# Kernel tuning notes

Measured on AMD Instinct MI355X. Metric: run time of the kernel, lower is better.

Reference implementation:

```python
import jax, jax.numpy as jnp
import numpy as np

B, N, DM, H = 2, 512, 1024, 16  # batch, seq, d_model, n_heads
DEPTHS = [1, 2, 4, 8]
LAM = 0.1  # lambda_distance


def setup_inputs() -> dict:
    key = jax.random.key(0)
    ks = jax.random.split(key, 2 + 5 * len(DEPTHS))
    inp = {
        "x": jax.random.normal(ks[0], (B, N, DM), jnp.float32),
        "depth_logits": jax.random.normal(ks[1], (len(DEPTHS),), jnp.float32),
    }
    j = 2
    for i, D in enumerate(DEPTHS):
        ds = DM // D
        r = max(1, D // 4)
        inp[f"pe{i}"] = jax.random.normal(ks[j], (N, D, ds), jnp.float32) * 0.02; j += 1
        inp[f"wqkv{i}"] = jax.random.normal(ks[j], (D, ds, 3 * ds), jnp.float32) / np.sqrt(ds); j += 1
        inp[f"wo{i}"] = jax.random.normal(ks[j], (DM, DM), jnp.float32) / np.sqrt(DM); j += 1
        inp[f"fu{i}"] = jax.random.normal(ks[j], (D, r), jnp.float32) / np.sqrt(r); j += 1
        inp[f"fv{i}"] = jax.random.normal(ks[j], (r, D), jnp.float32); j += 1
    return inp


def _ring_bias(n, lam, dtype):
    # toroidal (circular) distance bias on the sequence ring, normalized by N/2
    idx = jnp.arange(n)
    diff = jnp.abs(idx[:, None] - idx[None, :])
    ring = jnp.minimum(diff, n - diff).astype(dtype)
    return -lam * ring * (2.0 / n)  # [N, N]


def _toroidal_branch(x, pe, wqkv, wo, fu, fv):
    # x: [B, N, DM]; pe: [N, D, ds]; wqkv: [D, ds, 3ds]; wo: [DM, DM]; fu@fv: [D, D]
    b, n, dm = x.shape
    d_depth, ds, _ = wqkv.shape
    hd = ds // H
    xs = x.reshape(b, n, d_depth, ds) + pe[None]          # [B, N, D, ds]
    qkv = jnp.einsum('bnds,dse->bnde', xs, wqkv)          # per-depth-slice projection
    q, k, v = jnp.split(qkv, 3, axis=-1)
    q = q.reshape(b, n, d_depth, H, hd)
    k = k.reshape(b, n, d_depth, H, hd)
    v = v.reshape(b, n, d_depth, H, hd)
    bias = _ring_bias(n, LAM, x.dtype)
    scores = jnp.einsum('bndhe,bmdhe->bdhnm', q, k) / jnp.sqrt(jnp.asarray(hd, x.dtype))
    attn = jax.nn.softmax(scores + bias, axis=-1)          # [B, D, H, N, N]
    o = jnp.einsum('bdhnm,bmdhe->bndhe', attn, v).reshape(b, n, d_depth, ds)
    mix = fu @ fv                                          # low-rank depth fusion [D, D]
    fused = jnp.einsum('df,bnfs->bnds', mix, o).reshape(b, n, dm)
    return fused @ wo


def _forward(x, depth_logits, pe0, wqkv0, wo0, fu0, fv0, pe1, wqkv1, wo1, fu1, fv1,
             pe2, wqkv2, wo2, fu2, fv2, pe3, wqkv3, wo3, fu3, fv3):
    # inference-mode depth selection: hard one-hot at argmax (all branches still computed)
    w = jax.nn.one_hot(jnp.argmax(depth_logits), depth_logits.shape[0], dtype=x.dtype)
    params = [(pe0, wqkv0, wo0, fu0, fv0), (pe1, wqkv1, wo1, fu1, fv1),
              (pe2, wqkv2, wo2, fu2, fv2), (pe3, wqkv3, wo3, fu3, fv3)]
    out = jnp.zeros_like(x)
    for i, p in enumerate(params):
        out = out + w[i] * _toroidal_branch(x, *p)
    return out


def reference(x, depth_logits, pe0, wqkv0, wo0, fu0, fv0, pe1, wqkv1, wo1, fu1, fv1,
              pe2, wqkv2, wo2, fu2, fv2, pe3, wqkv3, wo3, fu3, fv3):
    return _forward(x, depth_logits, pe0, wqkv0, wo0, fu0, fv0, pe1, wqkv1, wo1, fu1, fv1,
                    pe2, wqkv2, wo2, fu2, fv2, pe3, wqkv3, wo3, fu3, fv3)
```

## Files before the change

### kernel.cpp

```cpp
#include <hip/hip_runtime.h>

#define B_   2
#define N_   512
#define DM_  1024
#define H_   16
#define LAM_ 0.1f

typedef __attribute__((ext_vector_type(8))) short bf16x8;
typedef __attribute__((ext_vector_type(4))) float f32x4;
typedef unsigned short ush;
struct ush4 { ush x, y, z, w; };
struct uint2s { unsigned x, y; };

__device__ inline ush f2bf(float v) {
    union { float f; unsigned u; } c; c.f = v;
    unsigned r = c.u + 0x7FFF + ((c.u >> 16) & 1);
    return (ush)(r >> 16);
}
__device__ inline float bf2f(ush b) {
    union { float f; unsigned u; } c; c.u = ((unsigned)b) << 16; return c.f;
}
__device__ inline f32x4 mfma16(bf16x8 a, bf16x8 b, f32x4 c) {
    return __builtin_amdgcn_mfma_f32_16x16x32_bf16(a, b, c, 0, 0, 0);
}

__global__ void k_select(const float* __restrict__ logits, int* __restrict__ sel) {
    if (threadIdx.x == 0) {
        float best = logits[0]; int bi = 0;
        for (int i = 1; i < 4; ++i) { float v = logits[i]; if (v > best) { best = v; bi = i; } }
        *sel = bi;
    }
}

template<int D>
__device__ void prep_wt_tile(int bT, int tid, const float* __restrict__ w,
                             ush* __restrict__ wh, ush* __restrict__ wl,
                             float (*lds)[65]) {
    constexpr int ds = DM_ / D;
    constexpr int tpr = 3 * ds / 64;
    constexpr int tpc = ds / 64;
    constexpr int tpd = tpr * tpc;
    if (bT >= D * tpd) return;
    const int d = bT / tpd, rem = bT % tpd;
    const int tr = rem / tpr, tc = rem % tpr;
    const float* src = w + (size_t)d * ds * 3 * ds;
    ush* dsth = wh + (size_t)d * 3 * ds * ds;
    ush* dstl = wl + (size_t)d * 3 * ds * ds;
    const int c = tid & 63, r0 = tid >> 6;
    #pragma unroll
    for (int j = 0; j < 16; ++j) {
        const int r = j * 4 + r0;
        lds[r][c] = src[(size_t)(tr * 64 + r) * (3 * ds) + tc * 64 + c];
    }
    __syncthreads();
    #pragma unroll
    for (int j = 0; j < 16; ++j) {
        const int r = j * 4 + r0;
        const float v = lds[c][r];
        const size_t o = (size_t)(tc * 64 + r) * ds + tr * 64 + c;
        const ush h = f2bf(v);
        dsth[o] = h; dstl[o] = f2bf(v - bf2f(h));
    }
}
__global__ __launch_bounds__(256) void k_prep(
        const int* __restrict__ sel, const float* __restrict__ x,
        const float* __restrict__ pe0, const float* __restrict__ pe1,
        const float* __restrict__ pe2, const float* __restrict__ pe3,
        const float* __restrict__ w0, const float* __restrict__ w1,
        const float* __restrict__ w2, const float* __restrict__ w3,
        const float* __restrict__ wo0, const float* __restrict__ wo1,
        const float* __restrict__ wo2, const float* __restrict__ wo3,
        ush* __restrict__ xh, ush* __restrict__ xl,
        ush* __restrict__ wqh, ush* __restrict__ wql,
        ush* __restrict__ woh, ush* __restrict__ wol) {
    __shared__ float lds[64][65];
    const int s = *sel;
    const int bid = blockIdx.x, tid = threadIdx.x;
    if (bid < 1024) {
        const float* pe = (s == 0) ? pe0 : (s == 1) ? pe1 : (s == 2) ? pe2 : pe3;
        const size_t i0 = ((size_t)bid * 256 + tid) * 4;
        const float4 xv = *(const float4*)&x[i0];
        const float4 pv = *(const float4*)&pe[i0 & ((size_t)N_ * DM_ - 1)];
        ush4 h4, l4;
        float v;
        v = xv.x + pv.x; h4.x = f2bf(v); l4.x = f2bf(v - bf2f(h4.x));
        v = xv.y + pv.y; h4.y = f2bf(v); l4.y = f2bf(v - bf2f(h4.y));
        v = xv.z + pv.z; h4.z = f2bf(v); l4.z = f2bf(v - bf2f(h4.z));
        v = xv.w + pv.w; h4.w = f2bf(v); l4.w = f2bf(v - bf2f(h4.w));
        *(ush4*)&xh[i0] = h4;
        *(ush4*)&xl[i0] = l4;
    } else if (bid < 1792) {
        const int bT = bid - 1024;
        switch (s) {
            case 0: prep_wt_tile<1>(bT, tid, w0, wqh, wql, lds); break;
            case 1: prep_wt_tile<2>(bT, tid, w1, wqh, wql, lds); break;
            case 2: prep_wt_tile<4>(bT, tid, w2, wqh, wql, lds); break;
            case 3: prep_wt_tile<8>(bT, tid, w3, wqh, wql, lds); break;
        }
    } else {
        const float* w = (s == 0) ? wo0 : (s == 1) ? wo1 : (s == 2) ? wo2 : wo3;
        const int bT = bid - 1792;
        const int tr = bT >> 4, tc = bT & 15;
        const int c = tid & 63, r0 = tid >> 6;
        #pragma unroll
        for (int j = 0; j < 16; ++j) {
            const int r = j * 4 + r0;
            lds[r][c] = w[(size_t)(tr * 64 + r) * DM_ + tc * 64 + c];
        }
        __syncthreads();
        #pragma unroll
        for (int j = 0; j < 16; ++j) {
            const int r = j * 4 + r0;
            const float v = lds[c][r];
            const size_t o = (size_t)(tc * 64 + r) * DM_ + tr * 64 + c;
            const ush h = f2bf(v);
            woh[o] = h; wol[o] = f2bf(v - bf2f(h));
        }
    }
}

template<int KD>
__device__ void gemm_core(const ush* __restrict__ Ah, const ush* __restrict__ Al, int lda,
                          const ush* __restrict__ Bh, const ush* __restrict__ Bl, int ldb,
                          int row0, int col0, int tid, ush* lds, f32x4 acc[2][2]) {
    ush* lAh = lds; ush* lAl = lds + 2560; ush* lBh = lds + 5120; ush* lBl = lds + 7680;
    const int srow = tid >> 2, scg = tid & 3;
    const int lane = tid & 63, w = tid >> 6;
    const int wm = w >> 1, wn = w & 1;
    const int lr = lane & 15, lb = lane >> 4;

    for (int k0 = 0; k0 < KD; k0 += 32) {
        *(bf16x8*)&lAh[srow * 40 + scg * 8] =
            *(const bf16x8*)&Ah[(size_t)(row0 + srow) * lda + k0 + scg * 8];
        *(bf16x8*)&lAl[srow * 40 + scg * 8] =
            *(const bf16x8*)&Al[(size_t)(row0 + srow) * lda + k0 + scg * 8];
        *(bf16x8*)&lBh[srow * 40 + scg * 8] =
            *(const bf16x8*)&Bh[(size_t)(col0 + srow) * ldb + k0 + scg * 8];
        *(bf16x8*)&lBl[srow * 40 + scg * 8] =
            *(const bf16x8*)&Bl[(size_t)(col0 + srow) * ldb + k0 + scg * 8];
        __syncthreads();
        bf16x8 ah[2], al[2], bh[2], bl[2];
        #pragma unroll
        for (int mg = 0; mg < 2; ++mg) {
            const int r = wm * 32 + mg * 16 + lr;
            ah[mg] = *(const bf16x8*)&lAh[r * 40 + lb * 8];
            al[mg] = *(const bf16x8*)&lAl[r * 40 + lb * 8];
        }
        #pragma unroll
        for (int ng = 0; ng < 2; ++ng) {
            const int r = wn * 32 + ng * 16 + lr;
            bh[ng] = *(const bf16x8*)&lBh[r * 40 + lb * 8];
            bl[ng] = *(const bf16x8*)&lBl[r * 40 + lb * 8];
        }
        #pragma unroll
        for (int mg = 0; mg < 2; ++mg)
            #pragma unroll
            for (int ng = 0; ng < 2; ++ng) {
                acc[mg][ng] = mfma16(ah[mg], bh[ng], acc[mg][ng]);
                acc[mg][ng] = mfma16(al[mg], bh[ng], acc[mg][ng]);
                acc[mg][ng] = mfma16(ah[mg], bl[ng], acc[mg][ng]);
            }
        __syncthreads();
    }
}

template<int D>
__device__ void qkv_body(int bid, int tid,
                         const ush* __restrict__ xh, const ush* __restrict__ xl,
                         const ush* __restrict__ wh, const ush* __restrict__ wl,
                         ush* __restrict__ Qh, ush* __restrict__ Ql,
                         ush* __restrict__ Kh, ush* __restrict__ Kl,
                         ush* __restrict__ Vth, ush* __restrict__ Vtl, ush* lds) {
    constexpr int ds = DM_ / D;
    constexpr int hd = ds / H_;
    constexpr int nx = 3 * ds / 64;
    const int bx = bid % nx, by = (bid / nx) & 7, bz = bid / (nx * 8);
    const int b = bz / D, d = bz % D;
    const int row0 = by * 64, col0 = bx * 64;

    f32x4 acc[2][2] = {};
    gemm_core<ds>(xh + (size_t)b * N_ * DM_ + d * ds, xl + (size_t)b * N_ * DM_ + d * ds, DM_,
                  wh + (size_t)d * 3 * ds * ds, wl + (size_t)d * 3 * ds * ds, ds,
                  row0, col0, tid, lds, acc);

    const int lane = tid & 63, w = tid >> 6;
    const int wm = w >> 1, wn = w & 1;
    const int lr = lane & 15, lb = lane >> 4;
    #pragma unroll
    for (int mg = 0; mg < 2; ++mg)
        #pragma unroll
        for (int ng = 0; ng < 2; ++ng) {
            const int n0 = row0 + wm * 32 + mg * 16 + lb * 4;
            const int e  = col0 + wn * 32 + ng * 16 + lr;
            const int part = e / ds, ep = e % ds;
            const int h = ep / hd, t = ep % hd;
            const size_t head = ((size_t)b * D + d) * H_ + h;
            if (part == 2) {
                ush4 h4, l4;
                const float v0 = acc[mg][ng][0], v1 = acc[mg][ng][1];
                const float v2 = acc[mg][ng][2], v3 = acc[mg][ng][3];
                h4.x = f2bf(v0); l4.x = f2bf(v0 - bf2f(h4.x));
                h4.y = f2bf(v1); l4.y = f2bf(v1 - bf2f(h4.y));
                h4.z = f2bf(v2); l4.z = f2bf(v2 - bf2f(h4.z));
                h4.w = f2bf(v3); l4.w = f2bf(v3 - bf2f(h4.w));
                const size_t o = (head * hd + t) * N_ + n0;
                *(ush4*)&Vth[o] = h4;
                *(ush4*)&Vtl[o] = l4;
            } else {
                #pragma unroll
                for (int i = 0; i < 4; ++i) {
                    const size_t o = (head * N_ + n0 + i) * hd + t;
                    const float v = acc[mg][ng][i];
                    const ush hh = f2bf(v), ll = f2bf(v - bf2f(hh));
                    if (part == 0) { Qh[o] = hh; Ql[o] = ll; }
                    else           { Kh[o] = hh; Kl[o] = ll; }
                }
            }
        }
}
__global__ __launch_bounds__(256) void k_qkv(
        const int* __restrict__ sel,
        const ush* __restrict__ xh, const ush* __restrict__ xl,
        const ush* __restrict__ wh, const ush* __restrict__ wl,
        ush* __restrict__ Qh, ush* __restrict__ Ql,
        ush* __restrict__ Kh, ush* __restrict__ Kl,
        ush* __restrict__ Vth, ush* __restrict__ Vtl) {
    __shared__ ush lds[4 * 2560];
    const int bid = blockIdx.x, tid = threadIdx.x;
    switch (*sel) {
        case 0: qkv_body<1>(bid, tid, xh, xl, wh, wl, Qh, Ql, Kh, Kl, Vth, Vtl, lds); break;
        case 1: qkv_body<2>(bid, tid, xh, xl, wh, wl, Qh, Ql, Kh, Kl, Vth, Vtl, lds); break;
        case 2: qkv_body<4>(bid, tid, xh, xl, wh, wl, Qh, Ql, Kh, Kl, Vth, Vtl, lds); break;
        case 3: qkv_body<8>(bid, tid, xh, xl, wh, wl, Qh, Ql, Kh, Kl, Vth, Vtl, lds); break;
    }
}

template<int D>
__device__ void attn_body(int bid, int tid,
        const ush* __restrict__ Qh, const ush* __restrict__ Ql,
        const ush* __restrict__ Kh, const ush* __restrict__ Kl,
        const ush* __restrict__ Vth, const ush* __restrict__ Vtl,
        float* __restrict__ O, ush* Pbase) {
    constexpr int ds = DM_ / D, hd = ds / H_;
    constexpr int CH = (hd >= 64) ? 2 : 1;
    constexpr int NT = (hd >= 16) ? hd / 16 : 1;
    constexpr int NBLK = B_ * D * H_ * 8;
    if (bid >= NBLK) return;
    const int bidr = (bid & 7) * (NBLK / 8) + (bid >> 3);
    const int w = tid >> 6;
    const int gw = bidr * 4 + w;
    const int head = gw >> 5, qt = gw & 31;
    const int h = head % H_, d = (head / H_) % D, b = head / (H_ * D);
    const int q0 = qt * 16;
    const size_t hb = (size_t)head * N_ * hd;
    const int lane = tid & 63;
    const int lr = lane & 15, lb = lane >> 4;
    ush* P = Pbase + w * 2048;
    const float L2E = 1.44269504f;
    const float SC  = rsqrtf((float)hd) * L2E;
    const float RB2 = LAM_ * (2.0f / N_) * L2E;
    const bf16x8 z8 = {0, 0, 0, 0, 0, 0, 0, 0};

    bf16x8 qah[CH], qal[CH];
    #pragma unroll
    for (int c = 0; c < CH; ++c) {
        const int k0 = c * 32 + lb * 8;
        bf16x8 vh = z8, vl = z8;
        if (k0 < hd) {
            const size_t o = hb + (size_t)(q0 + lr) * hd + k0;
            vh = *(const bf16x8*)&Qh[o];
            vl = *(const bf16x8*)&Ql[o];
        }
        qah[c] = vh; qal[c] = vl;
    }

    const int q = q0 + lr;
    float ls = 0.f;
    f32x4 acc2[NT];
    #pragma unroll
    for (int tt = 0; tt < NT; ++tt) acc2[tt] = (f32x4){0.f, 0.f, 0.f, 0.f};

    for (int pass = 0; pass < 4; ++pass) {
        const int col0 = pass * 128;

        f32x4 s[8];
        #pragma unroll
        for (int t = 0; t < 8; ++t) {
            const int kj0 = col0 + t * 16;
            f32x4 acc = {0.f, 0.f, 0.f, 0.f};
            #pragma unroll
            for (int c = 0; c < CH; ++c) {
                const int k0 = c * 32 + lb * 8;
                bf16x8 kh8 = z8, kl8 = z8;
                if (k0 < hd) {
                    const size_t o = hb + (size_t)(kj0 + lr) * hd + k0;
                    kh8 = *(const bf16x8*)&Kh[o];
                    kl8 = *(const bf16x8*)&Kl[o];
                }
                acc = mfma16(kh8, qah[c], acc);
                acc = mfma16(kl8, qah[c], acc);
                acc = mfma16(kh8, qal[c], acc);
            }
            s[t] = acc;
        }

        #pragma unroll
        for (int t = 0; t < 8; ++t) {
            const int kbase = col0 + t * 16 + lb * 4;
            float p[4];
            #pragma unroll
            for (int i = 0; i < 4; ++i) {
                int dd = q - (kbase + i); dd = dd < 0 ? -dd : dd;
                const int ring = (dd < N_ - dd) ? dd : (N_ - dd);
                p[i] = exp2f(s[t][i] * SC - RB2 * (float)ring);
            }
            unsigned pk0, pk1;
            asm("v_cvt_pk_bf16_f32 %0, %1, %2" : "=v"(pk0) : "v"(p[0]), "v"(p[1]));
            asm("v_cvt_pk_bf16_f32 %0, %1, %2" : "=v"(pk1) : "v"(p[2]), "v"(p[3]));
            union { unsigned u; float f; } c0, c1, c2, c3;
            c0.u = pk0 << 16; c1.u = pk0 & 0xffff0000u;
            c2.u = pk1 << 16; c3.u = pk1 & 0xffff0000u;
            ls += (c0.f + c1.f) + (c2.f + c3.f);
            const int off = ((lr << 8) + ((t * 16 + lb * 4) << 1)) ^ ((lr & 7) << 4);
            uint2s pv; pv.x = pk0; pv.y = pk1;
            *(uint2s*)((char*)P + off) = pv;
        }

        #pragma unroll
        for (int jc = 0; jc < 4; ++jc) {
            int poff = ((lr << 8) + ((jc * 32 + lb * 8) << 1)) ^ ((lr & 7) << 4);
            const bf16x8 pa = *(const bf16x8*)((const char*)P + poff);
            #pragma unroll
            for (int tt = 0; tt < NT; ++tt) {
                const size_t o = hb + (size_t)(tt * 16 + lr) * N_ + col0 + jc * 32 + lb * 8;
                const bf16x8 vh8 = *(const bf16x8*)&Vth[o];
                const bf16x8 vl8 = *(const bf16x8*)&Vtl[o];
                acc2[tt] = mfma16(pa, vh8, acc2[tt]);
                acc2[tt] = mfma16(pa, vl8, acc2[tt]);
            }
        }
    }

    ls += __shfl_xor(ls, 16);
    ls += __shfl_xor(ls, 32);
    float linv[4];
    #pragma unroll
    for (int i = 0; i < 4; ++i) linv[i] = 1.0f / __shfl(ls, lb * 4 + i);

    #pragma unroll
    for (int tt = 0; tt < NT; ++tt)
        #pragma unroll
        for (int i = 0; i < 4; ++i) {
            const int rn = q0 + lb * 4 + i;
            const int tc = tt * 16 + lr;
            if (tc < hd)
                O[((size_t)b * N_ + rn) * DM_ + d * ds + h * hd + tc] = acc2[tt][i] * linv[i];
        }
}
__global__ __launch_bounds__(256) void k_attn(
        const int* __restrict__ sel,
        const ush* __restrict__ Qh, const ush* __restrict__ Ql,
        const ush* __restrict__ Kh, const ush* __restrict__ Kl,
        const ush* __restrict__ Vth, const ush* __restrict__ Vtl,
        float* __restrict__ O) {
    __shared__ __align__(16) ush P[4 * 16 * 128];
    const int bid = blockIdx.x, tid = threadIdx.x;
    switch (*sel) {
        case 0: attn_body<1>(bid, tid, Qh, Ql, Kh, Kl, Vth, Vtl, O, P); break;
        case 1: attn_body<2>(bid, tid, Qh, Ql, Kh, Kl, Vth, Vtl, O, P); break;
        case 2: attn_body<4>(bid, tid, Qh, Ql, Kh, Kl, Vth, Vtl, O, P); break;
        case 3: attn_body<8>(bid, tid, Qh, Ql, Kh, Kl, Vth, Vtl, O, P); break;
    }
}

template<int D>
__device__ void mix_body(int bid, int tid, const float* __restrict__ fu,
                         const float* __restrict__ fv, const float* __restrict__ O,
                         ush* __restrict__ Fh, ush* __restrict__ Fl, float* mixs) {
    constexpr int ds = DM_ / D;
    constexpr int R = (D / 4 > 0) ? (D / 4) : 1;
    if (tid < D * D) {
        const int d = tid / D, f = tid % D;
        float m = 0.f;
        #pragma unroll
        for (int rr = 0; rr < R; ++rr) m += fu[d * R + rr] * fv[rr * D + f];
        mixs[tid] = m;
    }
    __syncthreads();
    const size_t idx = (size_t)bid * 256 + tid;
    const int dm = (int)(idx % DM_);
    const size_t bn = idx / DM_;
    const int d = dm / ds, s0 = dm % ds;
    const float* Ob = O + bn * DM_ + s0;
    float acc = 0.f;
    #pragma unroll
    for (int f = 0; f < D; ++f) acc += mixs[d * D + f] * Ob[(size_t)f * ds];
    const ush hh = f2bf(acc);
    Fh[idx] = hh; Fl[idx] = f2bf(acc - bf2f(hh));
}
__global__ __launch_bounds__(256) void k_mix(
        const int* __restrict__ sel,
        const float* __restrict__ fu0, const float* __restrict__ fv0,
        const float* __restrict__ fu1, const float* __restrict__ fv1,
        const float* __restrict__ fu2, const float* __restrict__ fv2,
        const float* __restrict__ fu3, const float* __restrict__ fv3,
        const float* __restrict__ O, ush* __restrict__ Fh, ush* __restrict__ Fl) {
    __shared__ float mixs[64];
    const int bid = blockIdx.x, tid = threadIdx.x;
    switch (*sel) {
        case 0: mix_body<1>(bid, tid, fu0, fv0, O, Fh, Fl, mixs); break;
        case 1: mix_body<2>(bid, tid, fu1, fv1, O, Fh, Fl, mixs); break;
        case 2: mix_body<4>(bid, tid, fu2, fv2, O, Fh, Fl, mixs); break;
        case 3: mix_body<8>(bid, tid, fu3, fv3, O, Fh, Fl, mixs); break;
    }
}

__global__ __launch_bounds__(256) void k_wo(
        const ush* __restrict__ Fh, const ush* __restrict__ Fl,
        const ush* __restrict__ wh, const ush* __restrict__ wl,
        float* __restrict__ out) {
    __shared__ ush lA[2][32 * 40];
    __shared__ ush lB[2][64 * 40];
    const int tid = threadIdx.x;
    const int bx = blockIdx.x & 15, by = blockIdx.x >> 4;
    const int row0 = by * 32, col0 = bx * 64;
    const int lane = tid & 63, w = tid >> 6;
    const int wq = w >> 1, wn = w & 1;
    const int lr = lane & 15, lb = lane >> 4;
    f32x4 acc[2] = {};

    for (int k0 = 0; k0 < DM_; k0 += 32) {
        {
            const int half = tid >> 7, t2 = tid & 127;
            const int srow = t2 >> 2, scg = t2 & 3;
            const ush* src = half ? Fl : Fh;
            *(bf16x8*)&lA[half][srow * 40 + scg * 8] =
                *(const bf16x8*)&src[(size_t)(row0 + srow) * DM_ + k0 + scg * 8];
        }
        {
            const int srow = tid >> 2, scg = tid & 3;
            *(bf16x8*)&lB[0][srow * 40 + scg * 8] =
                *(const bf16x8*)&wh[(size_t)(col0 + srow) * DM_ + k0 + scg * 8];
            *(bf16x8*)&lB[1][srow * 40 + scg * 8] =
                *(const bf16x8*)&wl[(size_t)(col0 + srow) * DM_ + k0 + scg * 8];
        }
        __syncthreads();
        const int ar = wq * 16 + lr;
        const bf16x8 ah = *(const bf16x8*)&lA[0][ar * 40 + lb * 8];
        const bf16x8 al = *(const bf16x8*)&lA[1][ar * 40 + lb * 8];
        #pragma unroll
        for (int ng = 0; ng < 2; ++ng) {
            const int br = wn * 32 + ng * 16 + lr;
            const bf16x8 bh = *(const bf16x8*)&lB[0][br * 40 + lb * 8];
            const bf16x8 bl = *(const bf16x8*)&lB[1][br * 40 + lb * 8];
            acc[ng] = mfma16(ah, bh, acc[ng]);
            acc[ng] = mfma16(al, bh, acc[ng]);
            acc[ng] = mfma16(ah, bl, acc[ng]);
        }
        __syncthreads();
    }
    #pragma unroll
    for (int ng = 0; ng < 2; ++ng)
        #pragma unroll
        for (int i = 0; i < 4; ++i) {
            const int r = row0 + wq * 16 + lb * 4 + i;
            const int c = col0 + wn * 32 + ng * 16 + lr;
            out[(size_t)r * DM_ + c] = acc[ng][i];
        }
}

extern "C" void kernel_launch(void* const* d_in, const int* in_sizes, int n_in,
                              void* d_out, int out_size, void* d_ws, size_t ws_size,
                              hipStream_t stream) {
    const float* x      = (const float*)d_in[0];
    const float* logits = (const float*)d_in[1];
    float* out = (float*)d_out;

    char* p = (char*)d_ws;
    int* sel = (int*)p; p += 256;
    const size_t MB = 1024 * 1024;
    ush* Qh = (ush*)p; p += 2 * MB;
    ush* Ql = (ush*)p; p += 2 * MB;
    ush* Kh = (ush*)p; p += 2 * MB;
    ush* Kl = (ush*)p; p += 2 * MB;
    ush* Vth = (ush*)p; p += 2 * MB + 65536;
    ush* Vtl = (ush*)p; p += 2 * MB + 65536;
    float* O = (float*)p; p += 4 * MB;
    ush* xh = (ush*)p; p += 2 * MB;
    ush* xl = (ush*)p; p += 2 * MB;
    ush* wqh = (ush*)p; p += 6 * MB;
    ush* wql = (ush*)p; p += 6 * MB;
    ush* woh = (ush*)p; p += 2 * MB;
    ush* wol = (ush*)p; p += 2 * MB;
    ush* Fh = xh, *Fl = xl;

    k_select<<<1, 64, 0, stream>>>(logits, sel);
    k_prep<<<dim3(2048), dim3(256), 0, stream>>>(
        sel, x,
        (const float*)d_in[2], (const float*)d_in[7],
        (const float*)d_in[12], (const float*)d_in[17],
        (const float*)d_in[3], (const float*)d_in[8],
        (const float*)d_in[13], (const float*)d_in[18],
        (const float*)d_in[4], (const float*)d_in[9],
        (const float*)d_in[14], (const float*)d_in[19],
        xh, xl, wqh, wql, woh, wol);
    k_qkv<<<dim3(768), dim3(256), 0, stream>>>(sel, xh, xl, wqh, wql,
                                               Qh, Ql, Kh, Kl, Vth, Vtl);
    k_attn<<<dim3(2048), dim3(256), 0, stream>>>(sel, Qh, Ql, Kh, Kl, Vth, Vtl, O);
    k_mix<<<dim3(B_ * N_ * DM_ / 256), dim3(256), 0, stream>>>(
        sel,
        (const float*)d_in[5],  (const float*)d_in[6],
        (const float*)d_in[10], (const float*)d_in[11],
        (const float*)d_in[15], (const float*)d_in[16],
        (const float*)d_in[20], (const float*)d_in[21],
        O, Fh, Fl);
    k_wo<<<dim3(512), dim3(256), 0, stream>>>(Fh, Fl, woh, wol, out);
}
```

Before: 100.8 us.

## Fold softmax row-sum into PV MFMA via ones-padded V and specialize attention kernels

Pads each head's transposed V with an extra row of ones, written in the prep kernel, so the softmax denominator comes out of the PV MFMA instead of a separate shuffle reduction. The attention loop now processes 32-key chunks with a small per-wave LDS buffer instead of 128-key passes, which cuts register pressure and LDS use. It also splits attention into four depth-specialized kernels that exit early unless selected. In exchange it adds three extra kernel launches, one padded MFMA tile per chunk, and larger V buffers.

```diff
diff --git a/kernel.cpp b/kernel.cpp
--- a/kernel.cpp
+++ b/kernel.cpp
@@ -23,6 +23,8 @@
 __device__ inline f32x4 mfma16(bf16x8 a, bf16x8 b, f32x4 c) {
     return __builtin_amdgcn_mfma_f32_16x16x32_bf16(a, b, c, 0, 0, 0);
 }
+
+template<int HD> struct vpad_t { static constexpr int PT = (HD >= 16) ? HD + 16 : 16; };
 
 __global__ void k_select(const float* __restrict__ logits, int* __restrict__ sel) {
     if (threadIdx.x == 0) {
@@ -62,6 +64,25 @@
         dsth[o] = h; dstl[o] = f2bf(v - bf2f(h));
     }
 }
+template<int D>
+__device__ void prep_vpad(int bT, int tid, ush* __restrict__ Vth, ush* __restrict__ Vtl) {
+    constexpr int ds = DM_ / D, hd = ds / H_;
+    constexpr int PT = vpad_t<hd>::PT;
+    constexpr int NH = B_ * D * H_;
+    constexpr int PR = PT - hd;
+    constexpr int TOT = NH * PR * (N_ / 4);
+    const int g = bT * 256 + tid;
+    if (g >= TOT) return;
+    constexpr int perh = PR * (N_ / 4);
+    const int head = g / perh, rem = g % perh;
+    const int r = hd + rem / (N_ / 4), n4 = (rem % (N_ / 4)) * 4;
+    const size_t o = ((size_t)head * PT + r) * N_ + n4;
+    const ush one = (r == hd) ? (ush)0x3F80 : (ush)0;
+    ush4 hv; hv.x = one; hv.y = one; hv.z = one; hv.w = one;
+    ush4 zv; zv.x = 0; zv.y = 0; zv.z = 0; zv.w = 0;
+    *(ush4*)&Vth[o] = hv;
+    *(ush4*)&Vtl[o] = zv;
+}
 __global__ __launch_bounds__(256) void k_prep(
         const int* __restrict__ sel, const float* __restrict__ x,
         const float* __restrict__ pe0, const float* __restrict__ pe1,
@@ -72,7 +93,8 @@
         const float* __restrict__ wo2, const float* __restrict__ wo3,
         ush* __restrict__ xh, ush* __restrict__ xl,
         ush* __restrict__ wqh, ush* __restrict__ wql,
-        ush* __restrict__ woh, ush* __restrict__ wol) {
+        ush* __restrict__ woh, ush* __restrict__ wol,
+        ush* __restrict__ Vth, ush* __restrict__ Vtl) {
     __shared__ float lds[64][65];
     const int s = *sel;
     const int bid = blockIdx.x, tid = threadIdx.x;
@@ -97,7 +119,7 @@
             case 2: prep_wt_tile<4>(bT, tid, w2, wqh, wql, lds); break;
             case 3: prep_wt_tile<8>(bT, tid, w3, wqh, wql, lds); break;
         }
-    } else {
+    } else if (bid < 2048) {
         const float* w = (s == 0) ? wo0 : (s == 1) ? wo1 : (s == 2) ? wo2 : wo3;
         const int bT = bid - 1792;
         const int tr = bT >> 4, tc = bT & 15;
@@ -115,6 +137,14 @@
             const size_t o = (size_t)(tc * 64 + r) * DM_ + tr * 64 + c;
             const ush h = f2bf(v);
             woh[o] = h; wol[o] = f2bf(v - bf2f(h));
+        }
+    } else {
+        const int bT = bid - 2048;
+        switch (s) {
+            case 0: prep_vpad<1>(bT, tid, Vth, Vtl); break;
+            case 1: prep_vpad<2>(bT, tid, Vth, Vtl); break;
+            case 2: prep_vpad<4>(bT, tid, Vth, Vtl); break;
+            case 3: prep_vpad<8>(bT, tid, Vth, Vtl); break;
         }
     }
 }
@@ -173,6 +203,7 @@
                          ush* __restrict__ Vth, ush* __restrict__ Vtl, ush* lds) {
     constexpr int ds = DM_ / D;
     constexpr int hd = ds / H_;
+    constexpr int PT = vpad_t<hd>::PT;
     constexpr int nx = 3 * ds / 64;
     const int bx = bid % nx, by = (bid / nx) & 7, bz = bid / (nx * 8);
     const int b = bz / D, d = bz % D;
@@ -203,7 +234,7 @@
                 h4.y = f2bf(v1); l4.y = f2bf(v1 - bf2f(h4.y));
                 h4.z = f2bf(v2); l4.z = f2bf(v2 - bf2f(h4.z));
                 h4.w = f2bf(v3); l4.w = f2bf(v3 - bf2f(h4.w));
-                const size_t o = (head * hd + t) * N_ + n0;
+                const size_t o = (head * PT + t) * N_ + n0;
                 *(ush4*)&Vth[o] = h4;
                 *(ush4*)&Vtl[o] = l4;
             } else {
@@ -236,14 +267,17 @@
 }
 
 template<int D>
-__device__ void attn_body(int bid, int tid,
+__device__ void attn_dev(int bid, int tid,
         const ush* __restrict__ Qh, const ush* __restrict__ Ql,
         const ush* __restrict__ Kh, const ush* __restrict__ Kl,
         const ush* __restrict__ Vth, const ush* __restrict__ Vtl,
-        float* __restrict__ O, ush* Pbase) {
+        float* __restrict__ O, ush* Pall) {
     constexpr int ds = DM_ / D, hd = ds / H_;
-    constexpr int CH = (hd >= 64) ? 2 : 1;
-    constexpr int NT = (hd >= 16) ? hd / 16 : 1;
+    constexpr int CH  = (hd >= 64) ? 2 : 1;
+    constexpr int NTP = (hd >= 16) ? hd / 16 + 1 : 1;
+    constexpr int PT  = vpad_t<hd>::PT;
+    constexpr int TL  = hd / 16;
+    constexpr int LRL = hd % 16;
     constexpr int NBLK = B_ * D * H_ * 8;
     if (bid >= NBLK) return;
     const int bidr = (bid & 7) * (NBLK / 8) + (bid >> 3);
@@ -252,10 +286,10 @@
     const int head = gw >> 5, qt = gw & 31;
     const int h = head % H_, d = (head / H_) % D, b = head / (H_ * D);
     const int q0 = qt * 16;
-    const size_t hb = (size_t)head * N_ * hd;
-    const int lane = tid & 63;
-    const int lr = lane & 15, lb = lane >> 4;
-    ush* P = Pbase + w * 2048;
+    const size_t hbq = (size_t)head * N_ * hd;
+    const size_t hbv = (size_t)head * PT * N_;
+    const int lane = tid & 63, lr = lane & 15, lb = lane >> 4;
+    ush* Pc = Pall + w * 16 * 40;
     const float L2E = 1.44269504f;
     const float SC  = rsqrtf((float)hd) * L2E;
     const float RB2 = LAM_ * (2.0f / N_) * L2E;
@@ -267,7 +301,7 @@
         const int k0 = c * 32 + lb * 8;
         bf16x8 vh = z8, vl = z8;
         if (k0 < hd) {
-            const size_t o = hb + (size_t)(q0 + lr) * hd + k0;
+            const size_t o = hbq + (size_t)(q0 + lr) * hd + k0;
             vh = *(const bf16x8*)&Qh[o];
             vl = *(const bf16x8*)&Ql[o];
         }
@@ -275,80 +309,68 @@
     }
 
     const int q = q0 + lr;
-    float ls = 0.f;
-    f32x4 acc2[NT];
-    #pragma unroll
-    for (int tt = 0; tt < NT; ++tt) acc2[tt] = (f32x4){0.f, 0.f, 0.f, 0.f};
-
-    for (int pass = 0; pass < 4; ++pass) {
-        const int col0 = pass * 128;
-
-        f32x4 s[8];
-        #pragma unroll
-        for (int t = 0; t < 8; ++t) {
-            const int kj0 = col0 + t * 16;
-            f32x4 acc = {0.f, 0.f, 0.f, 0.f};
-            #pragma unroll
-            for (int c = 0; c < CH; ++c) {
-                const int k0 = c * 32 + lb * 8;
-                bf16x8 kh8 = z8, kl8 = z8;
-                if (k0 < hd) {
-                    const size_t o = hb + (size_t)(kj0 + lr) * hd + k0;
-                    kh8 = *(const bf16x8*)&Kh[o];
-                    kl8 = *(const bf16x8*)&Kl[o];
-                }
-                acc = mfma16(kh8, qah[c], acc);
-                acc = mfma16(kl8, qah[c], acc);
-                acc = mfma16(kh8, qal[c], acc);
+    f32x4 acc2[NTP];
+    #pragma unroll
+    for (int tt = 0; tt < NTP; ++tt) acc2[tt] = (f32x4){0.f, 0.f, 0.f, 0.f};
+
+    for (int ck = 0; ck < 16; ++ck) {
+        const int col0 = ck * 32;
+
+        f32x4 s0 = {0.f, 0.f, 0.f, 0.f}, s1 = {0.f, 0.f, 0.f, 0.f};
+        #pragma unroll
+        for (int c = 0; c < CH; ++c) {
+            const int k0 = c * 32 + lb * 8;
+            bf16x8 k0h = z8, k0l = z8, k1h = z8, k1l = z8;
+            if (k0 < hd) {
+                const size_t o0 = hbq + (size_t)(col0 + lr) * hd + k0;
+                const size_t o1 = hbq + (size_t)(col0 + 16 + lr) * hd + k0;
+                k0h = *(const bf16x8*)&Kh[o0]; k0l = *(const bf16x8*)&Kl[o0];
+                k1h = *(const bf16x8*)&Kh[o1]; k1l = *(const bf16x8*)&Kl[o1];
             }
-            s[t] = acc;
-        }
-
-        #pragma unroll
-        for (int t = 0; t < 8; ++t) {
+            s0 = mfma16(k0h, qah[c], s0);
+            s0 = mfma16(k0l, qah[c], s0);
+            s0 = mfma16(k0h, qal[c], s0);
+            s1 = mfma16(k1h, qah[c], s1);
+            s1 = mfma16(k1l, qah[c], s1);
+            s1 = mfma16(k1h, qal[c], s1);
+        }
+
+        #pragma unroll
+        for (int t = 0; t < 2; ++t) {
+            const f32x4 sv = t ? s1 : s0;
             const int kbase = col0 + t * 16 + lb * 4;
             float p[4];
             #pragma unroll
             for (int i = 0; i < 4; ++i) {
                 int dd = q - (kbase + i); dd = dd < 0 ? -dd : dd;
                 const int ring = (dd < N_ - dd) ? dd : (N_ - dd);
-                p[i] = exp2f(s[t][i] * SC - RB2 * (float)ring);
+                p[i] = exp2f(sv[i] * SC - RB2 * (float)ring);
             }
             unsigned pk0, pk1;
             asm("v_cvt_pk_bf16_f32 %0, %1, %2" : "=v"(pk0) : "v"(p[0]), "v"(p[1]));
             asm("v_cvt_pk_bf16_f32 %0, %1, %2" : "=v"(pk1) : "v"(p[2]), "v"(p[3]));
-            union { unsigned u; float f; } c0, c1, c2, c3;
-            c0.u = pk0 << 16; c1.u = pk0 & 0xffff0000u;
-            c2.u = pk1 << 16; c3.u = pk1 & 0xffff0000u;
-            ls += (c0.f + c1.f) + (c2.f + c3.f);
-            const int off = ((lr << 8) + ((t * 16 + lb * 4) << 1)) ^ ((lr & 7) << 4);
             uint2s pv; pv.x = pk0; pv.y = pk1;
-            *(uint2s*)((char*)P + off) = pv;
-        }
-
-        #pragma unroll
-        for (int jc = 0; jc < 4; ++jc) {
-            int poff = ((lr << 8) + ((jc * 32 + lb * 8) << 1)) ^ ((lr & 7) << 4);
-            const bf16x8 pa = *(const bf16x8*)((const char*)P + poff);
-            #pragma unroll
-            for (int tt = 0; tt < NT; ++tt) {
-                const size_t o = hb + (size_t)(tt * 16 + lr) * N_ + col0 + jc * 32 + lb * 8;
-                const bf16x8 vh8 = *(const bf16x8*)&Vth[o];
-                const bf16x8 vl8 = *(const bf16x8*)&Vtl[o];
-                acc2[tt] = mfma16(pa, vh8, acc2[tt]);
-                acc2[tt] = mfma16(pa, vl8, acc2[tt]);
-            }
-        }
-    }
-
-    ls += __shfl_xor(ls, 16);
-    ls += __shfl_xor(ls, 32);
+            *(uint2s*)((char*)Pc + lr * 80 + t * 32 + lb * 8) = pv;
+        }
+
+        const bf16x8 pa = *(const bf16x8*)((const char*)Pc + lr * 80 + lb * 16);
+        #pragma unroll
+        for (int tt = 0; tt < NTP; ++tt) {
+            const size_t o = hbv + (size_t)(tt * 16 + lr) * N_ + col0 + lb * 8;
+            const bf16x8 vh8 = *(const bf16x8*)&Vth[o];
+            const bf16x8 vl8 = *(const bf16x8*)&Vtl[o];
+            acc2[tt] = mfma16(pa, vh8, acc2[tt]);
+            acc2[tt] = mfma16(pa, vl8, acc2[tt]);
+        }
+    }
+
     float linv[4];
     #pragma unroll
-    for (int i = 0; i < 4; ++i) linv[i] = 1.0f / __shfl(ls, lb * 4 + i);
-
-    #pragma unroll
-    for (int tt = 0; tt < NT; ++tt)
+    for (int i = 0; i < 4; ++i)
+        linv[i] = 1.0f / __shfl(acc2[TL][i], (lane & 48) | LRL);
+
+    #pragma unroll
+    for (int tt = 0; tt < NTP; ++tt)
         #pragma unroll
         for (int i = 0; i < 4; ++i) {
             const int rn = q0 + lb * 4 + i;
@@ -357,21 +379,21 @@
                 O[((size_t)b * N_ + rn) * DM_ + d * ds + h * hd + tc] = acc2[tt][i] * linv[i];
         }
 }
-__global__ __launch_bounds__(256) void k_attn(
-        const int* __restrict__ sel,
-        const ush* __restrict__ Qh, const ush* __restrict__ Ql,
-        const ush* __restrict__ Kh, const ush* __restrict__ Kl,
-        const ush* __restrict__ Vth, const ush* __restrict__ Vtl,
-        float* __restrict__ O) {
-    __shared__ __align__(16) ush P[4 * 16 * 128];
-    const int bid = blockIdx.x, tid = threadIdx.x;
-    switch (*sel) {
-        case 0: attn_body<1>(bid, tid, Qh, Ql, Kh, Kl, Vth, Vtl, O, P); break;
-        case 1: attn_body<2>(bid, tid, Qh, Ql, Kh, Kl, Vth, Vtl, O, P); break;
-        case 2: attn_body<4>(bid, tid, Qh, Ql, Kh, Kl, Vth, Vtl, O, P); break;
-        case 3: attn_body<8>(bid, tid, Qh, Ql, Kh, Kl, Vth, Vtl, O, P); break;
-    }
-}
+#define DEF_ATTN(NAME, DD, BR)                                                \
+__global__ __launch_bounds__(256) void NAME(                                  \
+        const int* __restrict__ sel,                                          \
+        const ush* __restrict__ Qh, const ush* __restrict__ Ql,               \
+        const ush* __restrict__ Kh, const ush* __restrict__ Kl,               \
+        const ush* __restrict__ Vth, const ush* __restrict__ Vtl,             \
+        float* __restrict__ O) {                                              \
+    __shared__ __align__(16) ush Pc[4 * 16 * 40];                             \
+    if (*sel != BR) return;                                                   \
+    attn_dev<DD>(blockIdx.x, threadIdx.x, Qh, Ql, Kh, Kl, Vth, Vtl, O, Pc);   \
+}
+DEF_ATTN(k_attn_1, 1, 0)
+DEF_ATTN(k_attn_2, 2, 1)
+DEF_ATTN(k_attn_4, 4, 2)
+DEF_ATTN(k_attn_8, 8, 3)
 
 template<int D>
 __device__ void mix_body(int bid, int tid, const float* __restrict__ fu,
@@ -483,8 +505,8 @@
     ush* Ql = (ush*)p; p += 2 * MB;
     ush* Kh = (ush*)p; p += 2 * MB;
     ush* Kl = (ush*)p; p += 2 * MB;
-    ush* Vth = (ush*)p; p += 2 * MB + 65536;
-    ush* Vtl = (ush*)p; p += 2 * MB + 65536;
+    ush* Vth = (ush*)p; p += 4 * MB;
+    ush* Vtl = (ush*)p; p += 4 * MB;
     float* O = (float*)p; p += 4 * MB;
     ush* xh = (ush*)p; p += 2 * MB;
     ush* xl = (ush*)p; p += 2 * MB;
@@ -495,7 +517,7 @@
     ush* Fh = xh, *Fl = xl;
 
     k_select<<<1, 64, 0, stream>>>(logits, sel);
-    k_prep<<<dim3(2048), dim3(256), 0, stream>>>(
+    k_prep<<<dim3(3072), dim3(256), 0, stream>>>(
         sel, x,
         (const float*)d_in[2], (const float*)d_in[7],
         (const float*)d_in[12], (const float*)d_in[17],
@@ -503,10 +525,13 @@
         (const float*)d_in[13], (const float*)d_in[18],
         (const float*)d_in[4], (const float*)d_in[9],
         (const float*)d_in[14], (const float*)d_in[19],
-        xh, xl, wqh, wql, woh, wol);
+        xh, xl, wqh, wql, woh, wol, Vth, Vtl);
     k_qkv<<<dim3(768), dim3(256), 0, stream>>>(sel, xh, xl, wqh, wql,
                                                Qh, Ql, Kh, Kl, Vth, Vtl);
-    k_attn<<<dim3(2048), dim3(256), 0, stream>>>(sel, Qh, Ql, Kh, Kl, Vth, Vtl, O);
+    k_attn_1<<<dim3(256),  dim3(256), 0, stream>>>(sel, Qh, Ql, Kh, Kl, Vth, Vtl, O);
+    k_attn_2<<<dim3(512),  dim3(256), 0, stream>>>(sel, Qh, Ql, Kh, Kl, Vth, Vtl, O);
+    k_attn_4<<<dim3(1024), dim3(256), 0, stream>>>(sel, Qh, Ql, Kh, Kl, Vth, Vtl, O);
+    k_attn_8<<<dim3(2048), dim3(256), 0, stream>>>(sel, Qh, Ql, Kh, Kl, Vth, Vtl, O);
     k_mix<<<dim3(B_ * N_ * DM_ / 256), dim3(256), 0, stream>>>(
         sel,
         (const float*)d_in[5],  (const float*)d_in[6],
```

Result: faster. 98.13 us (-2.6%).
